# Performance work log

Hardware: AMD Instinct MI355X
Metric: run time of the kernel (lower is better)

Reference implementation:

```python
import jax, jax.numpy as jnp
import numpy as np

N_LAYERS = 4
D_IN = 64
D_OUT = 64
D_MODEL = 512
D_STATE = 256
RMIN, RMAX, MAX_PHASE = 0.8, 0.95, 2.0 * np.pi


def setup_inputs() -> dict:
    key = jax.random.key(0)
    rng = np.random.default_rng(0)
    B, L = 8, 2048
    u = jax.random.normal(key, (B, L, D_IN), dtype=jnp.float32)
    # encoder/decoder (nn.Linear, bias=False): weight shape [out, in]
    encoder_w = jnp.asarray(rng.standard_normal((D_MODEL, D_IN)) / np.sqrt(D_IN), jnp.float32)
    decoder_w = jnp.asarray(rng.standard_normal((D_OUT, D_MODEL)) / np.sqrt(D_MODEL), jnp.float32)
    # LRU params per block (standard ring init on eigenvalues)
    u1 = rng.uniform(size=(N_LAYERS, D_STATE))
    u2 = rng.uniform(size=(N_LAYERS, D_STATE))
    nu_log = jnp.asarray(np.log(-0.5 * np.log(u1 * (RMAX**2 - RMIN**2) + RMIN**2)), jnp.float32)
    theta_log = jnp.asarray(np.log(MAX_PHASE * u2), jnp.float32)
    B_re = jnp.asarray(rng.standard_normal((N_LAYERS, D_STATE, D_MODEL)) / np.sqrt(2 * D_MODEL), jnp.float32)
    B_im = jnp.asarray(rng.standard_normal((N_LAYERS, D_STATE, D_MODEL)) / np.sqrt(2 * D_MODEL), jnp.float32)
    C_re = jnp.asarray(rng.standard_normal((N_LAYERS, D_MODEL, D_STATE)) / np.sqrt(D_STATE), jnp.float32)
    C_im = jnp.asarray(rng.standard_normal((N_LAYERS, D_MODEL, D_STATE)) / np.sqrt(D_STATE), jnp.float32)
    D = jnp.asarray(rng.standard_normal((N_LAYERS, D_MODEL)), jnp.float32)
    # GLU feedforward: y = (x W1^T) * sigmoid(x W2^T)
    W1 = jnp.asarray(rng.standard_normal((N_LAYERS, D_MODEL, D_MODEL)) / np.sqrt(D_MODEL), jnp.float32)
    W2 = jnp.asarray(rng.standard_normal((N_LAYERS, D_MODEL, D_MODEL)) / np.sqrt(D_MODEL), jnp.float32)
    res_logit = jnp.full((N_LAYERS,), -1.0, jnp.float32)
    return dict(u=u, encoder_w=encoder_w, decoder_w=decoder_w, nu_log=nu_log,
                theta_log=theta_log, B_re=B_re, B_im=B_im, C_re=C_re, C_im=C_im,
                D=D, W1=W1, W2=W2, res_logit=res_logit)


def _lru(x, nu, th, Bre, Bim, Cre, Cim, Dv):
    # diagonal complex LRU: h_t = lam*h_{t-1} + gamma*B u_t ; y = Re(C h) + D*u
    lam = jnp.exp(-jnp.exp(nu) + 1j * jnp.exp(th)).astype(jnp.complex64)  # [N]
    gam = jnp.sqrt(1.0 - jnp.abs(lam) ** 2).astype(jnp.complex64)
    Bc = (Bre + 1j * Bim).astype(jnp.complex64)  # [N, D]
    Bu = jnp.einsum('bld,nd->bln', x.astype(jnp.complex64), Bc) * gam  # [B,L,N]
    lam_b = jnp.broadcast_to(lam, Bu.shape)

    def comb(a, b):
        return (a[0] * b[0], a[1] * b[0] + b[1])

    _, h = jax.lax.associative_scan(comb, (lam_b, Bu), axis=1)
    Cc = (Cre + 1j * Cim).astype(jnp.complex64)  # [D, N]
    return jnp.real(jnp.einsum('bln,dn->bld', h, Cc)) + Dv * x


def reference(u, encoder_w, decoder_w, nu_log, theta_log, B_re, B_im, C_re, C_im, D, W1, W2, res_logit):
    x = jnp.einsum('bli,mi->blm', u, encoder_w)  # encoder
    for k in range(N_LAYERS):
        z = _lru(x, nu_log[k], theta_log[k], B_re[k], B_im[k], C_re[k], C_im[k], D[k])
        z = jnp.einsum('bld,od->blo', z, W1[k]) * jax.nn.sigmoid(jnp.einsum('bld,od->blo', z, W2[k]))
        x = x + jax.nn.sigmoid(res_logit[k]) * z  # gated residual (dropout=0)
    return jnp.einsum('blm,om->blo', x, decoder_w)  # decoder
```

## Files before the change

### kernel.cpp

```cpp
#include <hip/hip_runtime.h>
#include <cmath>

#define DM 512
#define DS 256
#define NL 4
#define BATCH 8
#define SEQ 2048
#define MROWS (BATCH*SEQ)
#define LCH 32
#define NCH 64

typedef unsigned short ushort_t;
typedef unsigned int uint_t;
typedef __attribute__((ext_vector_type(8))) short short8;
typedef __attribute__((ext_vector_type(4))) float floatx4;

__device__ __forceinline__ float sigmoidf_(float v) { return 1.0f / (1.0f + __expf(-v)); }

__device__ __forceinline__ ushort_t f2bf(float f) {
    union { float f; unsigned int u; } c; c.f = f;
    unsigned int u = c.u;
    u += 0x7fffu + ((u >> 16) & 1u);
    return (ushort_t)(u >> 16);
}
__device__ __forceinline__ float bf2f(uint_t h) {
    union { unsigned int u; float f; } c; c.u = (h & 0xffffu) << 16; return c.f;
}
__device__ __forceinline__ uint_t pack2(float a, float b) {
    return (uint_t)f2bf(a) | ((uint_t)f2bf(b) << 16);
}

#define AS1 __attribute__((address_space(1)))
#define AS3 __attribute__((address_space(3)))
__device__ __forceinline__ void gl_lds16(const void* g, void* l) {
    __builtin_amdgcn_global_load_lds((const AS1 uint_t*)g, (AS3 uint_t*)l, 16, 0, 0);
}

struct GemmArgs {
    const ushort_t* A;
    const ushort_t* Wa;
    const ushort_t* Wb;
    const ushort_t* xbf_in;
    const float* gam;
    const float* Dv;
    float* of32;
    ushort_t* obf;
    const float* resp;
    int K;
    int N;
    int layer;
};

#define PREFETCH_TILE(it_, buf_)                                                        \
    do {                                                                                \
        const size_t kb_ = (size_t)(it_) * 64;                                          \
        char* dst_ = smem + (buf_) * HALF;                                              \
        gl_lds16(Ap + (size_t)(wid * 16 + lrow) * Kb + kb_, dst_ + wid * 1024);         \
        gl_lds16(Ap + (size_t)((wid + 4) * 16 + lrow) * Kb + kb_,                       \
                 dst_ + (wid + 4) * 1024);                                              \
        gl_lds16(B0p + (size_t)(wid * 16 + lrow) * Kb + kb_, dst_ + AB + wid * 1024);   \
        if constexpr (BN == 128) {                                                      \
            gl_lds16(B0p + (size_t)((wid + 4) * 16 + lrow) * Kb + kb_,                  \
                     dst_ + AB + (wid + 4) * 1024);                                     \
        }                                                                               \
        if constexpr (DUAL) {                                                           \
            gl_lds16(B1p + (size_t)(wid * 16 + lrow) * Kb + kb_,                        \
                     dst_ + AB + BB + wid * 1024);                                      \
            if constexpr (BN == 128) {                                                  \
                gl_lds16(B1p + (size_t)((wid + 4) * 16 + lrow) * Kb + kb_,              \
                         dst_ + AB + BB + (wid + 4) * 1024);                            \
            }                                                                           \
        }                                                                               \
    } while (0)

template<int BN, int EPI, int DUAL>
__launch_bounds__(256, DUAL ? 2 : 3)
__global__ void mgemm(const GemmArgs p) {
    constexpr int BM = 128;
    constexpr int MT = (BN == 128) ? 4 : 2;
    constexpr int NT = 4;
    constexpr int WROWS = MT * 16;
    constexpr int AB = 8192;
    constexpr int BB = (BN == 128) ? 8192 : 4096;
    constexpr int B1B = DUAL ? BB : 0;
    constexpr int HALF = AB + BB + B1B;
    constexpr int EPB = (EPI == 4) ? 0 : 32 * 132 * 4;
    constexpr int SMB = (2 * HALF > EPB) ? 2 * HALF : EPB;
    __shared__ __align__(16) char smem[SMB];

    const int K = p.K, N = p.N;
    const int tid = threadIdx.x, lane = tid & 63, wid = tid >> 6;
    const int wm = (BN == 128) ? (wid & 1) : wid;
    const int wn = (BN == 128) ? (wid >> 1) : 0;

    const int flat = blockIdx.y * 128 + blockIdx.x;
    const int xcd = flat & 7, sidx = flat >> 3;
    const int bx = xcd * 16 + (sidx & 15);
    const int by = sidx >> 4;

    const int m0 = bx * BM, n0 = by * BN;
    const int q = lane >> 4, r16 = lane & 15;
    const int lrow = lane >> 2;
    const size_t Kb = (size_t)K * 2;
    const char* Ap  = (const char*)p.A  + (size_t)m0 * Kb + (lane & 3) * 16;
    const char* B0p = (const char*)p.Wa + (size_t)n0 * Kb + (lane & 3) * 16;
    const char* B1p = (const char*)p.Wb + (size_t)n0 * Kb + (lane & 3) * 16;

    floatx4 acc0[MT][NT] = {};
    floatx4 acc1[DUAL ? MT : 1][DUAL ? NT : 1] = {};

    const int iters = K >> 5;
    PREFETCH_TILE(0, 0);
    for (int it = 0; it < iters; ++it) {
        __syncthreads();
        if (it + 1 < iters) PREFETCH_TILE(it + 1, (it + 1) & 1);
        const ushort_t* As  = (const ushort_t*)(smem + (it & 1) * HALF);
        const ushort_t* Bs0 = (const ushort_t*)(smem + (it & 1) * HALF + AB);
        const ushort_t* Bs1 = (const ushort_t*)(smem + (it & 1) * HALF + AB + BB);

        short8 af[MT], b0[NT], b1[DUAL ? NT : 1];
#pragma unroll
        for (int i = 0; i < MT; ++i)
            af[i] = *(const short8*)&As[(wm * WROWS + i * 16 + r16) * 32 + q * 8];
#pragma unroll
        for (int j = 0; j < NT; ++j) {
            b0[j] = *(const short8*)&Bs0[(wn * 64 + j * 16 + r16) * 32 + q * 8];
            if constexpr (DUAL)
                b1[j] = *(const short8*)&Bs1[(wn * 64 + j * 16 + r16) * 32 + q * 8];
        }
#pragma unroll
        for (int i = 0; i < MT; ++i)
#pragma unroll
            for (int j = 0; j < NT; ++j) {
                acc0[i][j] = __builtin_amdgcn_mfma_f32_16x16x32_bf16(af[i], b0[j], acc0[i][j], 0, 0, 0);
                if constexpr (DUAL)
                    acc1[i][j] = __builtin_amdgcn_mfma_f32_16x16x32_bf16(af[i], b1[j], acc1[i][j], 0, 0, 0);
            }
    }

    if constexpr (EPI == 4) {
#pragma unroll
        for (int i = 0; i < MT; ++i)
#pragma unroll
            for (int j = 0; j < NT; ++j)
#pragma unroll
                for (int rr = 0; rr < 4; ++rr) {
                    const int row = m0 + wm * WROWS + i * 16 + q * 4 + rr;
                    const int col = wn * 64 + j * 16 + r16;
                    p.of32[(size_t)row * N + col] = acc0[i][j][rr];
                }
        return;
    } else {
        float* eps = (float*)smem;
        float rsv = 0.f;
        if constexpr (EPI == 3) rsv = sigmoidf_(p.resp[p.layer]);

#pragma unroll
        for (int i = 0; i < MT; ++i) {
            __syncthreads();
#pragma unroll
            for (int j = 0; j < NT; ++j) {
                const int colt = wn * 64 + j * 16 + r16;
#pragma unroll
                for (int rr = 0; rr < 4; ++rr) {
                    float v = acc0[i][j][rr];
                    if constexpr (EPI == 1) v *= p.gam[(n0 + colt) >> 1];
                    if constexpr (EPI == 3) v = rsv * v * sigmoidf_(acc1[i][j][rr]);
                    eps[(wm * 16 + q * 4 + rr) * 132 + colt] = v;
                }
            }
            __syncthreads();
            const int row_r = tid >> 3, colg = (tid & 7) * 16;
            const int grow = m0 + (row_r >> 4) * 64 + i * 16 + (row_r & 15);
            const int gcol = n0 + colg;
            float4 f[4];
#pragma unroll
            for (int c = 0; c < 4; ++c) f[c] = *(float4*)&eps[row_r * 132 + colg + c * 4];
            const size_t ob = (size_t)grow * N + gcol;

            if constexpr (EPI == 2) {
                uint_t xp[8];
                *(uint4*)(xp)     = *(const uint4*)(p.xbf_in + ob);
                *(uint4*)(xp + 4) = *(const uint4*)(p.xbf_in + ob + 8);
#pragma unroll
                for (int c = 0; c < 4; ++c) {
                    float4 dv = *(const float4*)(p.Dv + gcol + c * 4);
                    f[c].x += dv.x * bf2f(xp[2 * c]);
                    f[c].y += dv.y * bf2f(xp[2 * c] >> 16);
                    f[c].z += dv.z * bf2f(xp[2 * c + 1]);
                    f[c].w += dv.w * bf2f(xp[2 * c + 1] >> 16);
                }
            } else if constexpr (EPI == 3) {
                uint_t xp[8];
                *(uint4*)(xp)     = *(const uint4*)(p.xbf_in + ob);
                *(uint4*)(xp + 4) = *(const uint4*)(p.xbf_in + ob + 8);
#pragma unroll
                for (int c = 0; c < 4; ++c) {
                    f[c].x += bf2f(xp[2 * c]);
                    f[c].y += bf2f(xp[2 * c] >> 16);
                    f[c].z += bf2f(xp[2 * c + 1]);
                    f[c].w += bf2f(xp[2 * c + 1] >> 16);
                }
            }
            uint4 p0, p1;
            p0.x = pack2(f[0].x, f[0].y); p0.y = pack2(f[0].z, f[0].w);
            p0.z = pack2(f[1].x, f[1].y); p0.w = pack2(f[1].z, f[1].w);
            p1.x = pack2(f[2].x, f[2].y); p1.y = pack2(f[2].z, f[2].w);
            p1.z = pack2(f[3].x, f[3].y); p1.w = pack2(f[3].z, f[3].w);
            *(uint4*)(p.obf + ob) = p0;
            *(uint4*)(p.obf + ob + 8) = p1;
        }
    }
}

__global__ void prep_all(const float* __restrict__ u, const float* __restrict__ enc,
                         const float* __restrict__ dec, const float* __restrict__ nu,
                         const float* __restrict__ th,
                         const float* __restrict__ Bre, const float* __restrict__ Bim,
                         const float* __restrict__ Cre, const float* __restrict__ Cim,
                         const float* __restrict__ W1, const float* __restrict__ W2,
                         ushort_t* __restrict__ WBb, ushort_t* __restrict__ Wzb,
                         ushort_t* __restrict__ W1b, ushort_t* __restrict__ W2b,
                         ushort_t* __restrict__ encb, ushort_t* __restrict__ decb,
                         ushort_t* __restrict__ ubf,
                         float* __restrict__ lre, float* __restrict__ lim,
                         float* __restrict__ gm) {
    const int idx = blockIdx.x * 256 + threadIdx.x;
    const int k = idx & 511, n = (idx >> 9) & 511, l = idx >> 18;
    {
        const int s = n >> 1, part = n & 1;
        const float* src = part ? Bim : Bre;
        WBb[idx] = f2bf(src[((size_t)l * DS + s) * DM + k]);
    }
    {
        const int s = k >> 1, part = k & 1;
        float v = part ? -Cim[((size_t)l * DM + n) * DS + s]
                       :  Cre[((size_t)l * DM + n) * DS + s];
        Wzb[idx] = f2bf(v);
    }
    W1b[idx] = f2bf(W1[idx]);
    W2b[idx] = f2bf(W2[idx]);
    ubf[idx] = f2bf(u[idx]);
    if (idx < DM * 64) { encb[idx] = f2bf(enc[idx]); decb[idx] = f2bf(dec[idx]); }
    if (idx < NL * DS) {
        float a = expf(-expf(nu[idx])), t = expf(th[idx]);
        lre[idx] = a * cosf(t);
        lim[idx] = a * sinf(t);
        gm[idx] = sqrtf(fmaxf(0.f, 1.f - a * a));
    }
}

__global__ __launch_bounds__(256) void scan_ends(
        const uint_t* __restrict__ Bu, const float* __restrict__ lre_,
        const float* __restrict__ lim_, float* __restrict__ carry) {
    const int s = threadIdx.x;
    const int blk = blockIdx.x, b = blk >> 6, c = blk & 63;
    const float lre = lre_[s], lim = lim_[s];
    float hre = 0.f, him = 0.f;
    size_t base = ((size_t)b * SEQ + (size_t)c * LCH) * DS + s;
#pragma unroll 8
    for (int i = 0; i < LCH; ++i, base += DS) {
        uint_t u = Bu[base];
        float br = bf2f(u), bi = bf2f(u >> 16);
        float nr = fmaf(lre, hre, fmaf(-lim, him, br));
        float ni = fmaf(lre, him, fmaf(lim, hre, bi));
        hre = nr; him = ni;
    }
    carry[(size_t)blk * 512 + s] = hre;
    carry[(size_t)blk * 512 + DS + s] = him;
}

__global__ __launch_bounds__(256) void scan_apply_lb(
        const uint_t* __restrict__ Bu, const float* __restrict__ lre_,
        const float* __restrict__ lim_, const float* __restrict__ carry,
        uint_t* __restrict__ h) {
    const int s = threadIdx.x;
    const int blk = blockIdx.x, b = blk >> 6, c = blk & 63;
    const float lre = lre_[s], lim = lim_[s];

    float gre = 0.f, gim = 0.f;
    if (c > 0) {
        float are = lre, aim = lim;
#pragma unroll
        for (int t = 0; t < 5; ++t) {
            float nr = are * are - aim * aim, ni = 2.f * are * aim;
            are = nr; aim = ni;
        }
        const int depth = (c < 12) ? c : 12;
        float pwr = 1.f, pwi = 0.f;
        for (int j = c - 1; j >= c - depth; --j) {
            const size_t jb = (size_t)(b * NCH + j) * 512 + s;
            float er = carry[jb], ei = carry[jb + DS];
            gre = fmaf(pwr, er, fmaf(-pwi, ei, gre));
            gim = fmaf(pwr, ei, fmaf(pwi, er, gim));
            float nr = pwr * are - pwi * aim, ni = pwr * aim + pwi * are;
            pwr = nr; pwi = ni;
        }
    }

    float hr = gre, hi = gim;
    size_t base = ((size_t)b * SEQ + (size_t)c * LCH) * DS + s;
#pragma unroll 8
    for (int i = 0; i < LCH; ++i, base += DS) {
        uint_t uu = Bu[base];
        float br = bf2f(uu), bi = bf2f(uu >> 16);
        float nr = fmaf(lre, hr, fmaf(-lim, hi, br));
        float ni = fmaf(lre, hi, fmaf(lim, hr, bi));
        hr = nr; hi = ni;
        h[base] = pack2(hr, hi);
    }
}

extern "C" void kernel_launch(void* const* d_in, const int* in_sizes, int n_in,
                              void* d_out, int out_size, void* d_ws, size_t ws_size,
                              hipStream_t stream) {
    const float* u   = (const float*)d_in[0];
    const float* enc = (const float*)d_in[1];
    const float* dec = (const float*)d_in[2];
    const float* nu  = (const float*)d_in[3];
    const float* th  = (const float*)d_in[4];
    const float* Bre = (const float*)d_in[5];
    const float* Bim = (const float*)d_in[6];
    const float* Cre = (const float*)d_in[7];
    const float* Cim = (const float*)d_in[8];
    const float* Dp  = (const float*)d_in[9];
    const float* W1  = (const float*)d_in[10];
    const float* W2  = (const float*)d_in[11];
    const float* res = (const float*)d_in[12];
    float* out = (float*)d_out;

    const size_t MD = (size_t)MROWS * DM;
    float* carry = (float*)d_ws;
    float* lre  = carry + (size_t)BATCH * NCH * 512;
    float* lim  = lre + NL * DS;
    float* gmt  = lim + NL * DS;
    ushort_t* xbf  = (ushort_t*)(gmt + NL * DS);
    ushort_t* Bubf = xbf + MD;
    ushort_t* hbf  = Bubf + MD;
    ushort_t* zbf  = hbf + MD;
    ushort_t* ubf  = zbf;
    ushort_t* WBb  = zbf + MD;
    ushort_t* Wzb  = WBb + (size_t)NL * DM * DM;
    ushort_t* W1b  = Wzb + (size_t)NL * DM * DM;
    ushort_t* W2b  = W1b + (size_t)NL * DM * DM;
    ushort_t* encb = W2b + (size_t)NL * DM * DM;
    ushort_t* decb = encb + DM * 64;

    prep_all<<<NL * DM * DM / 256, 256, 0, stream>>>(
        u, enc, dec, nu, th, Bre, Bim, Cre, Cim, W1, W2,
        WBb, Wzb, W1b, W2b, encb, decb, ubf, lre, lim, gmt);

    const dim3 gFull(MROWS / 128, DM / 128);

    {
        GemmArgs a = {};
        a.A = ubf; a.Wa = encb; a.K = 64; a.N = DM;
        a.obf = xbf;
        mgemm<128, 0, 0><<<gFull, 256, 0, stream>>>(a);
    }

    for (int k = 0; k < NL; ++k) {
        {
            GemmArgs a = {};
            a.A = xbf; a.Wa = WBb + (size_t)k * DM * DM; a.K = DM; a.N = DM;
            a.obf = Bubf; a.gam = gmt + k * DS;
            mgemm<128, 1, 0><<<gFull, 256, 0, stream>>>(a);
        }
        scan_ends<<<BATCH * NCH, 256, 0, stream>>>((const uint_t*)Bubf,
                                                   lre + k * DS, lim + k * DS, carry);
        scan_apply_lb<<<BATCH * NCH, 256, 0, stream>>>((const uint_t*)Bubf,
                                                       lre + k * DS, lim + k * DS, carry,
                                                       (uint_t*)hbf);
        {
            GemmArgs a = {};
            a.A = hbf; a.Wa = Wzb + (size_t)k * DM * DM; a.K = DM; a.N = DM;
            a.obf = zbf; a.xbf_in = xbf; a.Dv = Dp + k * DM;
            mgemm<128, 2, 0><<<gFull, 256, 0, stream>>>(a);
        }
        {
            GemmArgs a = {};
            a.A = zbf; a.Wa = W1b + (size_t)k * DM * DM; a.Wb = W2b + (size_t)k * DM * DM;
            a.K = DM; a.N = DM;
            a.obf = xbf; a.xbf_in = xbf; a.resp = res; a.layer = k;
            mgemm<128, 3, 1><<<gFull, 256, 0, stream>>>(a);
        }
    }
    {
        GemmArgs a = {};
        a.A = xbf; a.Wa = decb; a.K = DM; a.N = 64;
        a.of32 = out;
        mgemm<64, 4, 0><<<dim3(MROWS / 128, 1), 256, 0, stream>>>(a);
    }
}
```

Before: 388.5 us.

## Fuse chunk-end scan carries into Bu GEMM epilogue, drop scan_ends kernel

The Bu projection GEMM epilogue now stages its bf16 output tile in shared memory and runs the per-chunk local recurrence there, writing chunk-end carries directly. This removes the separate scan_ends kernel and its re-read of the Bu buffer for each layer. It enlarges the epilogue shared memory for that variant, which may reduce occupancy, and it drops the XCD-aware block index remapping for all GEMMs, which may hurt L2 locality.

New measurement: 369.6 us. 1.05x faster.

```diff
diff --git a/kernel.cpp b/kernel.cpp
--- a/kernel.cpp
+++ b/kernel.cpp
@@ -46,6 +46,9 @@
     float* of32;
     ushort_t* obf;
     const float* resp;
+    const float* lamre;
+    const float* lamim;
+    float* carry;
     int K;
     int N;
     int layer;
@@ -84,7 +87,9 @@
     constexpr int BB = (BN == 128) ? 8192 : 4096;
     constexpr int B1B = DUAL ? BB : 0;
     constexpr int HALF = AB + BB + B1B;
-    constexpr int EPB = (EPI == 4) ? 0 : 32 * 132 * 4;
+    constexpr int EPB = (EPI == 4) ? 0
+                      : (EPI == 1) ? (32 * 132 * 4 + 128 * 66 * 4)
+                      : 32 * 132 * 4;
     constexpr int SMB = (2 * HALF > EPB) ? 2 * HALF : EPB;
     __shared__ __align__(16) char smem[SMB];
 
@@ -92,13 +97,7 @@
     const int tid = threadIdx.x, lane = tid & 63, wid = tid >> 6;
     const int wm = (BN == 128) ? (wid & 1) : wid;
     const int wn = (BN == 128) ? (wid >> 1) : 0;
-
-    const int flat = blockIdx.y * 128 + blockIdx.x;
-    const int xcd = flat & 7, sidx = flat >> 3;
-    const int bx = xcd * 16 + (sidx & 15);
-    const int by = sidx >> 4;
-
-    const int m0 = bx * BM, n0 = by * BN;
+    const int m0 = blockIdx.x * BM, n0 = blockIdx.y * BN;
     const int q = lane >> 4, r16 = lane & 15;
     const int lrow = lane >> 2;
     const size_t Kb = (size_t)K * 2;
@@ -152,6 +151,7 @@
         return;
     } else {
         float* eps = (float*)smem;
+        uint_t* zst = (uint_t*)(smem + 32 * 132 * 4);
         float rsv = 0.f;
         if constexpr (EPI == 3) rsv = sigmoidf_(p.resp[p.layer]);
 
@@ -171,7 +171,8 @@
             }
             __syncthreads();
             const int row_r = tid >> 3, colg = (tid & 7) * 16;
-            const int grow = m0 + (row_r >> 4) * 64 + i * 16 + (row_r & 15);
+            const int lr = (row_r >> 4) * 64 + i * 16 + (row_r & 15);
+            const int grow = m0 + lr;
             const int gcol = n0 + colg;
             float4 f[4];
 #pragma unroll
@@ -209,6 +210,31 @@
             p1.z = pack2(f[3].x, f[3].y); p1.w = pack2(f[3].z, f[3].w);
             *(uint4*)(p.obf + ob) = p0;
             *(uint4*)(p.obf + ob + 8) = p1;
+            if constexpr (EPI == 1) {
+                const int c0 = colg >> 1;
+                *(uint4*)&zst[lr * 66 + c0]     = p0;
+                *(uint4*)&zst[lr * 66 + c0 + 4] = p1;
+            }
+        }
+
+        if constexpr (EPI == 1) {
+            __syncthreads();
+            const int c4 = tid >> 6, s6 = tid & 63;
+            const int sg = (n0 >> 1) + s6;
+            const float lr_ = p.lamre[sg], li_ = p.lamim[sg];
+            float hr = 0.f, hi = 0.f;
+#pragma unroll 8
+            for (int i2 = 0; i2 < LCH; ++i2) {
+                uint_t uu = zst[(c4 * LCH + i2) * 66 + s6];
+                float br = bf2f(uu), bi = bf2f(uu >> 16);
+                float nr = fmaf(lr_, hr, fmaf(-li_, hi, br));
+                float ni = fmaf(lr_, hi, fmaf(li_, hr, bi));
+                hr = nr; hi = ni;
+            }
+            const int b = m0 >> 11;
+            const int cblk = ((m0 & (SEQ - 1)) >> 5) + c4;
+            const size_t cb = (size_t)(b * NCH + cblk) * 512 + sg;
+            p.carry[cb] = hr; p.carry[cb + DS] = hi;
         }
     }
 }
@@ -250,26 +276,6 @@
     }
 }
 
-__global__ __launch_bounds__(256) void scan_ends(
-        const uint_t* __restrict__ Bu, const float* __restrict__ lre_,
-        const float* __restrict__ lim_, float* __restrict__ carry) {
-    const int s = threadIdx.x;
-    const int blk = blockIdx.x, b = blk >> 6, c = blk & 63;
-    const float lre = lre_[s], lim = lim_[s];
-    float hre = 0.f, him = 0.f;
-    size_t base = ((size_t)b * SEQ + (size_t)c * LCH) * DS + s;
-#pragma unroll 8
-    for (int i = 0; i < LCH; ++i, base += DS) {
-        uint_t u = Bu[base];
-        float br = bf2f(u), bi = bf2f(u >> 16);
-        float nr = fmaf(lre, hre, fmaf(-lim, him, br));
-        float ni = fmaf(lre, him, fmaf(lim, hre, bi));
-        hre = nr; him = ni;
-    }
-    carry[(size_t)blk * 512 + s] = hre;
-    carry[(size_t)blk * 512 + DS + s] = him;
-}
-
 __global__ __launch_bounds__(256) void scan_apply_lb(
         const uint_t* __restrict__ Bu, const float* __restrict__ lre_,
         const float* __restrict__ lim_, const float* __restrict__ carry,
@@ -364,10 +370,9 @@
             GemmArgs a = {};
             a.A = xbf; a.Wa = WBb + (size_t)k * DM * DM; a.K = DM; a.N = DM;
             a.obf = Bubf; a.gam = gmt + k * DS;
+            a.lamre = lre + k * DS; a.lamim = lim + k * DS; a.carry = carry;
             mgemm<128, 1, 0><<<gFull, 256, 0, stream>>>(a);
         }
-        scan_ends<<<BATCH * NCH, 256, 0, stream>>>((const uint_t*)Bubf,
-                                                   lre + k * DS, lim + k * DS, carry);
         scan_apply_lb<<<BATCH * NCH, 256, 0, stream>>>((const uint_t*)Bubf,
                                                        lre + k * DS, lim + k * DS, carry,
                                                        (uint_t*)hbf);
```
